# Performance work log

Measured on AMD Instinct MI355X. Metric: run time of the kernel, lower is better.

The kernel has to match this reference:

```python
import jax, jax.numpy as jnp
import numpy as np

N_LEADS = 12

def _norm_adj():
    """Normalized adjacency matching GCNConv semantics on the fixed ECG graph.
    The buffer adj already includes eye(12); PyG GCNConv (add_self_loops=True)
    adds one more self-loop of weight 1, so effective self-weight is 2.
    A_norm = D^{-1/2} A_eff D^{-1/2}.
    """
    adj = np.zeros((N_LEADS, N_LEADS), dtype=np.float32)
    conns = [(0, 1), (0, 2), (1, 2), (0, 3), (1, 3), (2, 3), (0, 4), (1, 4), (1, 5), (2, 5),
             (6, 7), (7, 8), (8, 9), (9, 10), (10, 11)]
    for i, j in conns:
        adj[i, j] = 1.0
        adj[j, i] = 1.0
    a_eff = adj + 2.0 * np.eye(N_LEADS, dtype=np.float32)  # buffer eye + PyG self-loop
    deg = a_eff.sum(axis=1)
    dinv = 1.0 / np.sqrt(deg)
    return jnp.asarray(dinv[:, None] * a_eff * dinv[None, :])

A_NORM = _norm_adj()  # (12, 12)

def setup_inputs() -> dict:
    key = jax.random.key(0)
    ks = jax.random.split(key, 7)
    B, F_IN, H, OUT = 16384, 512, 256, 128
    s = 0.02
    return {
        "x": jax.random.normal(ks[0], (B, N_LEADS, F_IN), dtype=jnp.float32),
        "W1": jax.random.normal(ks[1], (F_IN, H), dtype=jnp.float32) * s,
        "b1": jnp.zeros((H,), dtype=jnp.float32),
        "W2": jax.random.normal(ks[2], (H, H), dtype=jnp.float32) * s,
        "b2": jnp.zeros((H,), dtype=jnp.float32),
        "W3": jax.random.normal(ks[3], (H, OUT), dtype=jnp.float32) * s,
        "b3": jnp.zeros((OUT,), dtype=jnp.float32),
    }

def _gcn(a, x, w, b):
    # GCNConv: A_norm @ (X W) + b, batched over b. Shapes: x (B,12,f), w (f,o)
    return jnp.einsum("nm,bmo->bno", a, jnp.einsum("bnf,fo->bno", x, w)) + b

def reference(x, W1, b1, W2, b2, W3, b3):
    a = A_NORM.astype(x.dtype)
    h = jax.nn.relu(_gcn(a, x, W1, b1))   # dropout is identity in eval mode
    h = jax.nn.relu(_gcn(a, h, W2, b2))
    h = _gcn(a, h, W3, b3)                # (B, 12, out)
    x_mean = h.mean(axis=1)
    x_max = h.max(axis=1)
    return jnp.concatenate([x_mean, x_max], axis=1)  # (B, 2*out)
```

## Files before the change

kernel.cpp:

```cpp
#include <hip/hip_runtime.h>
#include <math.h>

typedef _Float16 f16x8 __attribute__((ext_vector_type(8)));
typedef _Float16 f16x2 __attribute__((ext_vector_type(2)));
typedef float    f32x4 __attribute__((ext_vector_type(4)));

namespace {
constexpr unsigned kMask[12] = {0x01Eu,0x03Du,0x02Bu,0x007u,0x003u,0x006u,
                                0x080u,0x140u,0x280u,0x500u,0xA00u,0x400u};
constexpr float kDinv[12] = {
    0.40824829046386302f, 0.37796447300922720f, 0.40824829046386302f,
    0.44721359549995794f, 0.5f, 0.5f,
    0.57735026918962576f, 0.5f, 0.5f, 0.5f, 0.5f, 0.57735026918962576f};

constexpr int ROWS = 48;
constexpr int AST  = 72;
constexpr int HST  = 258;
constexpr int ABYTES = ROWS * AST * 2;
constexpr int HBYTES = ROWS * HST * 2;
constexpr int SMEM   = ABYTES + HBYTES;
}

__device__ __forceinline__ void barrier_keep_vmcnt()
{
    __builtin_amdgcn_sched_barrier(0);
    asm volatile("s_waitcnt lgkmcnt(0)" ::: "memory");
    __builtin_amdgcn_s_barrier();
    __builtin_amdgcn_sched_barrier(0);
}

template<int R0>
__device__ __forceinline__ void mix_rows(const float2 (&y)[12],
                                         _Float16* __restrict__ Abuf,
                                         int g, int f2)
{
    #pragma unroll
    for (int i = 0; i < 3; ++i) {
        const int r = R0 + i;
        float sx = 2.0f * y[r].x;
        float sy = 2.0f * y[r].y;
        #pragma unroll
        for (int j = 0; j < 12; ++j)
            if ((kMask[r] >> j) & 1u) { sx += y[j].x; sy += y[j].y; }
        sx *= kDinv[r]; sy *= kDinv[r];
        f16x2 h2; h2.x = (_Float16)sx; h2.y = (_Float16)sy;
        *(f16x2*)&Abuf[(g*12 + r)*AST + f2*2] = h2;
    }
}

template<int K, int N, bool SRC_LDS>
__device__ __forceinline__ void run_layer(
    const float*    __restrict__ xg,
    const _Float16* __restrict__ hs,
    const _Float16* __restrict__ wt,
    _Float16* __restrict__ Abuf,
    long rowbase, int tid,
    f32x4 (&acc)[3][N/128])
{
    constexpr int NT = N / 128, KC = K / 64;
    const int lane = tid & 63, wave = tid >> 6;
    const int l15 = lane & 15, q = lane >> 4;
    const int g   = (tid >> 5) & 3;
    const int f2  = tid & 31;
    const int qtr = tid >> 7;

    #pragma unroll
    for (int a = 0; a < 3; ++a)
        #pragma unroll
        for (int b = 0; b < NT; ++b)
            acc[a][b] = (f32x4){0.f, 0.f, 0.f, 0.f};

    float2 y[12];
    if constexpr (!SRC_LDS) {
        #pragma unroll
        for (int n = 0; n < 12; ++n) {
            const float* p = xg + (rowbase + g*12 + n) * (long)K + f2*2;
            y[n].x = kDinv[n] * p[0]; y[n].y = kDinv[n] * p[1];
        }
    }

    for (int kc = 0; kc < KC; ++kc) {
        f16x8 bf[2][NT];
        #pragma unroll
        for (int ks = 0; ks < 2; ++ks)
            #pragma unroll
            for (int tn = 0; tn < NT; ++tn)
                bf[ks][tn] = *(const f16x8*)(wt
                    + (long)(wave*NT*16 + tn*16 + l15) * K
                    + kc*64 + ks*32 + q*8);

        if constexpr (SRC_LDS) {
            #pragma unroll
            for (int n = 0; n < 12; ++n) {
                const f16x2 h2 = *(const f16x2*)&hs[(g*12 + n)*HST + kc*64 + f2*2];
                y[n].x = kDinv[n] * (float)h2.x;
                y[n].y = kDinv[n] * (float)h2.y;
            }
        }
        switch (qtr) {
            case 0:  mix_rows<0>(y, Abuf, g, f2); break;
            case 1:  mix_rows<3>(y, Abuf, g, f2); break;
            case 2:  mix_rows<6>(y, Abuf, g, f2); break;
            default: mix_rows<9>(y, Abuf, g, f2); break;
        }

        if constexpr (!SRC_LDS) {
            if (kc + 1 < KC) {
                #pragma unroll
                for (int n = 0; n < 12; ++n) {
                    const float* p = xg + (rowbase + g*12 + n) * (long)K
                                        + (kc + 1)*64 + f2*2;
                    y[n].x = kDinv[n] * p[0]; y[n].y = kDinv[n] * p[1];
                }
            }
        }
        barrier_keep_vmcnt();

        #pragma unroll
        for (int ks = 0; ks < 2; ++ks) {
            f16x8 af[3];
            #pragma unroll
            for (int tm = 0; tm < 3; ++tm)
                af[tm] = *(const f16x8*)&Abuf[(tm*16 + l15)*AST + ks*32 + q*8];
            #pragma unroll
            for (int tm = 0; tm < 3; ++tm)
                #pragma unroll
                for (int tn = 0; tn < NT; ++tn)
                    acc[tm][tn] = __builtin_amdgcn_mfma_f32_16x16x32_f16(
                        af[tm], bf[ks][tn], acc[tm][tn], 0, 0, 0);
        }
        barrier_keep_vmcnt();
    }
}

template<int N>
__device__ __forceinline__ void store_h(
    f32x4 (&acc)[3][N/128], const float* __restrict__ bias,
    _Float16* __restrict__ H, int tid)
{
    constexpr int NT = N / 128;
    const int lane = tid & 63, wave = tid >> 6;
    const int l15 = lane & 15, q = lane >> 4;
    float bcol[NT];
    #pragma unroll
    for (int tn = 0; tn < NT; ++tn) bcol[tn] = bias[wave*NT*16 + tn*16 + l15];
    #pragma unroll
    for (int tm = 0; tm < 3; ++tm)
        #pragma unroll
        for (int tn = 0; tn < NT; ++tn)
            #pragma unroll
            for (int r = 0; r < 4; ++r) {
                const int row = tm*16 + q*4 + r;
                const int col = wave*NT*16 + tn*16 + l15;
                H[row*HST + col] = (_Float16)fmaxf(acc[tm][tn][r] + bcol[tn], 0.f);
            }
}

__global__ __launch_bounds__(512, 4)
void gcn_fused(const float* __restrict__ x,
               const _Float16* __restrict__ wt1, const float* __restrict__ b1,
               const _Float16* __restrict__ wt2, const float* __restrict__ b2,
               const _Float16* __restrict__ wt3, const float* __restrict__ b3,
               float* __restrict__ out)
{
    __shared__ __align__(16) char smem[SMEM];
    _Float16* Abuf = (_Float16*)smem;
    _Float16* Hbuf = (_Float16*)(smem + ABYTES);

    const int tid = threadIdx.x;
    const long rowbase = (long)blockIdx.x * ROWS;

    f32x4 acc[3][2];
    run_layer<512, 256, false>(x, nullptr, wt1, Abuf, rowbase, tid, acc);
    store_h<256>(acc, b1, Hbuf, tid);
    __syncthreads();

    run_layer<256, 256, true>(nullptr, Hbuf, wt2, Abuf, rowbase, tid, acc);
    store_h<256>(acc, b2, Hbuf, tid);
    __syncthreads();

    f32x4 acc3[3][1];
    run_layer<256, 128, true>(nullptr, Hbuf, wt3, Abuf, rowbase, tid, acc3);

    float* C = (float*)smem;
    {
        const int lane = tid & 63, wave = tid >> 6;
        const int l15 = lane & 15, q = lane >> 4;
        #pragma unroll
        for (int tm = 0; tm < 3; ++tm)
            #pragma unroll
            for (int r = 0; r < 4; ++r) {
                const int row = tm*16 + q*4 + r;
                const int col = wave*16 + l15;
                C[row*129 + col] = acc3[tm][0][r];
            }
    }
    __syncthreads();
    {
        const int bl  = tid >> 7;
        const int col = tid & 127;
        float s = 0.0f, mx = -INFINITY;
        #pragma unroll
        for (int n = 0; n < 12; ++n) {
            const float v = C[(bl*12 + n)*129 + col];
            s += v; mx = fmaxf(mx, v);
        }
        const float b  = b3[col];
        const long  ob = ((long)blockIdx.x*4 + bl) * 256;
        out[ob + col]       = s / 12.0f + b;
        out[ob + 128 + col] = mx + b;
    }
}

__global__ void prep_weights(const float* __restrict__ W1,
                             const float* __restrict__ W2,
                             const float* __restrict__ W3,
                             _Float16* __restrict__ wt)
{
    const int tid = blockIdx.x * 256 + threadIdx.x;
    constexpr int N1 = 512*256, N2 = 256*256, N3 = 256*128;
    if (tid < N1) {
        const int o = tid >> 9, k = tid & 511;
        wt[tid] = (_Float16)W1[k*256 + o];
    } else if (tid < N1 + N2) {
        const int t = tid - N1;
        const int o = t >> 8, k = t & 255;
        wt[N1 + t] = (_Float16)W2[k*256 + o];
    } else if (tid < N1 + N2 + N3) {
        const int t = tid - N1 - N2;
        const int o = t >> 8, k = t & 255;
        wt[N1 + N2 + t] = (_Float16)W3[k*128 + o];
    }
}

extern "C" void kernel_launch(void* const* d_in, const int* in_sizes, int n_in,
                              void* d_out, int out_size, void* d_ws, size_t ws_size,
                              hipStream_t stream)
{
    const float* x  = (const float*)d_in[0];
    const float* W1 = (const float*)d_in[1];
    const float* b1 = (const float*)d_in[2];
    const float* W2 = (const float*)d_in[3];
    const float* b2 = (const float*)d_in[4];
    const float* W3 = (const float*)d_in[5];
    const float* b3 = (const float*)d_in[6];
    float* out = (float*)d_out;

    _Float16* wt  = (_Float16*)d_ws;
    _Float16* wt1 = wt;
    _Float16* wt2 = wt + 512*256;
    _Float16* wt3 = wt + 512*256 + 256*256;

    prep_weights<<<896, 256, 0, stream>>>(W1, W2, W3, wt);
    gcn_fused<<<4096, 512, 0, stream>>>(x, wt1, b1, wt2, b2, wt3, b3, out);
}
```

Before: 745.5 us.

## Double-buffer A tiles, double rows per block, split graph mixing by component

New measurement: 602.2 us. 1.24x faster.

```diff
diff --git a/kernel.cpp b/kernel.cpp
--- a/kernel.cpp
+++ b/kernel.cpp
@@ -6,17 +6,16 @@
 typedef float    f32x4 __attribute__((ext_vector_type(4)));
 
 namespace {
-constexpr unsigned kMask[12] = {0x01Eu,0x03Du,0x02Bu,0x007u,0x003u,0x006u,
-                                0x080u,0x140u,0x280u,0x500u,0xA00u,0x400u};
 constexpr float kDinv[12] = {
     0.40824829046386302f, 0.37796447300922720f, 0.40824829046386302f,
     0.44721359549995794f, 0.5f, 0.5f,
     0.57735026918962576f, 0.5f, 0.5f, 0.5f, 0.5f, 0.57735026918962576f};
 
-constexpr int ROWS = 48;
-constexpr int AST  = 72;
-constexpr int HST  = 258;
-constexpr int ABYTES = ROWS * AST * 2;
+constexpr int ROWS  = 96;
+constexpr int AST   = 72;
+constexpr int AHALF = ROWS * AST;
+constexpr int ABYTES = 2 * AHALF * 2;
+constexpr int HST   = 258;
 constexpr int HBYTES = ROWS * HST * 2;
 constexpr int SMEM   = ABYTES + HBYTES;
 }
@@ -29,129 +28,177 @@
     __builtin_amdgcn_sched_barrier(0);
 }
 
-template<int R0>
-__device__ __forceinline__ void mix_rows(const float2 (&y)[12],
-                                         _Float16* __restrict__ Abuf,
-                                         int g, int f2)
-{
-    #pragma unroll
-    for (int i = 0; i < 3; ++i) {
-        const int r = R0 + i;
-        float sx = 2.0f * y[r].x;
-        float sy = 2.0f * y[r].y;
-        #pragma unroll
-        for (int j = 0; j < 12; ++j)
-            if ((kMask[r] >> j) & 1u) { sx += y[j].x; sy += y[j].y; }
-        sx *= kDinv[r]; sy *= kDinv[r];
-        f16x2 h2; h2.x = (_Float16)sx; h2.y = (_Float16)sy;
-        *(f16x2*)&Abuf[(g*12 + r)*AST + f2*2] = h2;
-    }
+template<int K, bool SRC_LDS, bool CB>
+__device__ __forceinline__ void load_y(const float* __restrict__ xrow,
+                                       const _Float16* __restrict__ hs,
+                                       int g, int f2, int kc, float2 (&y)[6])
+{
+    #pragma unroll
+    for (int n = 0; n < 6; ++n) {
+        const float d = kDinv[(CB ? 6 : 0) + n];
+        if constexpr (!SRC_LDS) {
+            const float* p = xrow + (long)n * K + kc * 64;
+            y[n].x = d * p[0];
+            y[n].y = d * p[1];
+        } else {
+            const f16x2 h2 = *(const f16x2*)&hs[(g*12 + (CB?6:0) + n)*HST + kc*64 + f2*2];
+            y[n].x = d * (float)h2.x;
+            y[n].y = d * (float)h2.y;
+        }
+    }
+}
+
+template<bool CB>
+__device__ __forceinline__ void mix6(const float2 (&y)[6],
+                                     _Float16* __restrict__ A, int g, int f2)
+{
+    float rx[6], ry[6];
+    if constexpr (!CB) {
+        rx[0] = 2.f*y[0].x + y[1].x + y[2].x + y[3].x + y[4].x;
+        ry[0] = 2.f*y[0].y + y[1].y + y[2].y + y[3].y + y[4].y;
+        rx[1] = 2.f*y[1].x + y[0].x + y[2].x + y[3].x + y[4].x + y[5].x;
+        ry[1] = 2.f*y[1].y + y[0].y + y[2].y + y[3].y + y[4].y + y[5].y;
+        rx[2] = 2.f*y[2].x + y[0].x + y[1].x + y[3].x + y[5].x;
+        ry[2] = 2.f*y[2].y + y[0].y + y[1].y + y[3].y + y[5].y;
+        rx[3] = 2.f*y[3].x + y[0].x + y[1].x + y[2].x;
+        ry[3] = 2.f*y[3].y + y[0].y + y[1].y + y[2].y;
+        rx[4] = 2.f*y[4].x + y[0].x + y[1].x;
+        ry[4] = 2.f*y[4].y + y[0].y + y[1].y;
+        rx[5] = 2.f*y[5].x + y[1].x + y[2].x;
+        ry[5] = 2.f*y[5].y + y[1].y + y[2].y;
+    } else {
+        rx[0] = 2.f*y[0].x + y[1].x;
+        ry[0] = 2.f*y[0].y + y[1].y;
+        rx[1] = 2.f*y[1].x + y[0].x + y[2].x;
+        ry[1] = 2.f*y[1].y + y[0].y + y[2].y;
+        rx[2] = 2.f*y[2].x + y[1].x + y[3].x;
+        ry[2] = 2.f*y[2].y + y[1].y + y[3].y;
+        rx[3] = 2.f*y[3].x + y[2].x + y[4].x;
+        ry[3] = 2.f*y[3].y + y[2].y + y[4].y;
+        rx[4] = 2.f*y[4].x + y[3].x + y[5].x;
+        ry[4] = 2.f*y[4].y + y[3].y + y[5].y;
+        rx[5] = 2.f*y[5].x + y[4].x;
+        ry[5] = 2.f*y[5].y + y[4].y;
+    }
+    #pragma unroll
+    for (int i = 0; i < 6; ++i) {
+        const float d = kDinv[(CB ? 6 : 0) + i];
+        f16x2 h2;
+        h2.x = (_Float16)(d * rx[i]);
+        h2.y = (_Float16)(d * ry[i]);
+        *(f16x2*)&A[(g*12 + (CB?6:0) + i)*AST + f2*2] = h2;
+    }
+}
+
+template<int K, int N, bool SRC_LDS>
+__device__ __forceinline__ void layer_iter(
+    const float* __restrict__ xrow, const _Float16* __restrict__ hs,
+    const _Float16* __restrict__ wtl,
+    const _Float16* __restrict__ AbufR, _Float16* __restrict__ AbufW,
+    bool cb, int g, int f2, int kc, int l15, int q,
+    float2 (&yCons)[6], float2 (&yFill)[6],
+    f32x4 (&acc)[6][N/128])
+{
+    constexpr int NTW = N / 128, KC = K / 64;
+
+    f16x8 bf[2][NTW];
+    #pragma unroll
+    for (int ks = 0; ks < 2; ++ks)
+        #pragma unroll
+        for (int tn = 0; tn < NTW; ++tn)
+            bf[ks][tn] = *(const f16x8*)(wtl + (long)tn*16*K + kc*64 + ks*32);
+
+    if (cb) {
+        if constexpr (!SRC_LDS)
+            if (kc + 2 < KC) load_y<K,false,true>(xrow, hs, g, f2, kc+2, yFill);
+        if (kc + 1 < KC) {
+            if constexpr (SRC_LDS) load_y<K,true,true>(xrow, hs, g, f2, kc+1, yCons);
+            mix6<true>(yCons, AbufW, g, f2);
+        }
+    } else {
+        if constexpr (!SRC_LDS)
+            if (kc + 2 < KC) load_y<K,false,false>(xrow, hs, g, f2, kc+2, yFill);
+        if (kc + 1 < KC) {
+            if constexpr (SRC_LDS) load_y<K,true,false>(xrow, hs, g, f2, kc+1, yCons);
+            mix6<false>(yCons, AbufW, g, f2);
+        }
+    }
+
+    #pragma unroll
+    for (int ks = 0; ks < 2; ++ks)
+        #pragma unroll
+        for (int tm = 0; tm < 6; ++tm) {
+            const f16x8 af = *(const f16x8*)&AbufR[(tm*16 + l15)*AST + ks*32 + q*8];
+            #pragma unroll
+            for (int tn = 0; tn < NTW; ++tn)
+                acc[tm][tn] = __builtin_amdgcn_mfma_f32_16x16x32_f16(
+                    af, bf[ks][tn], acc[tm][tn], 0, 0, 0);
+        }
+    barrier_keep_vmcnt();
 }
 
 template<int K, int N, bool SRC_LDS>
 __device__ __forceinline__ void run_layer(
-    const float*    __restrict__ xg,
-    const _Float16* __restrict__ hs,
-    const _Float16* __restrict__ wt,
-    _Float16* __restrict__ Abuf,
-    long rowbase, int tid,
-    f32x4 (&acc)[3][N/128])
-{
-    constexpr int NT = N / 128, KC = K / 64;
+    const float* __restrict__ xg, const _Float16* __restrict__ hs,
+    const _Float16* __restrict__ wt, _Float16* __restrict__ Abuf,
+    long rowbase, int tid, f32x4 (&acc)[6][N/128])
+{
+    constexpr int NTW = N / 128, KC = K / 64;
     const int lane = tid & 63, wave = tid >> 6;
     const int l15 = lane & 15, q = lane >> 4;
-    const int g   = (tid >> 5) & 3;
-    const int f2  = tid & 31;
-    const int qtr = tid >> 7;
-
-    #pragma unroll
-    for (int a = 0; a < 3; ++a)
-        #pragma unroll
-        for (int b = 0; b < NT; ++b)
+    const bool cb = tid >= 256;
+    const int mi = tid & 255, g = mi >> 5, f2 = mi & 31;
+
+    const float* xrow = nullptr;
+    if constexpr (!SRC_LDS)
+        xrow = xg + (rowbase + g*12 + (cb ? 6 : 0)) * (long)K + f2*2;
+    const _Float16* wtl = wt + (long)(wave*NTW*16 + l15) * K + q*8;
+
+    #pragma unroll
+    for (int a = 0; a < 6; ++a)
+        #pragma unroll
+        for (int b = 0; b < NTW; ++b)
             acc[a][b] = (f32x4){0.f, 0.f, 0.f, 0.f};
 
-    float2 y[12];
-    if constexpr (!SRC_LDS) {
-        #pragma unroll
-        for (int n = 0; n < 12; ++n) {
-            const float* p = xg + (rowbase + g*12 + n) * (long)K + f2*2;
-            y[n].x = kDinv[n] * p[0]; y[n].y = kDinv[n] * p[1];
-        }
-    }
-
-    for (int kc = 0; kc < KC; ++kc) {
-        f16x8 bf[2][NT];
-        #pragma unroll
-        for (int ks = 0; ks < 2; ++ks)
-            #pragma unroll
-            for (int tn = 0; tn < NT; ++tn)
-                bf[ks][tn] = *(const f16x8*)(wt
-                    + (long)(wave*NT*16 + tn*16 + l15) * K
-                    + kc*64 + ks*32 + q*8);
-
-        if constexpr (SRC_LDS) {
-            #pragma unroll
-            for (int n = 0; n < 12; ++n) {
-                const f16x2 h2 = *(const f16x2*)&hs[(g*12 + n)*HST + kc*64 + f2*2];
-                y[n].x = kDinv[n] * (float)h2.x;
-                y[n].y = kDinv[n] * (float)h2.y;
-            }
-        }
-        switch (qtr) {
-            case 0:  mix_rows<0>(y, Abuf, g, f2); break;
-            case 1:  mix_rows<3>(y, Abuf, g, f2); break;
-            case 2:  mix_rows<6>(y, Abuf, g, f2); break;
-            default: mix_rows<9>(y, Abuf, g, f2); break;
-        }
-
-        if constexpr (!SRC_LDS) {
-            if (kc + 1 < KC) {
-                #pragma unroll
-                for (int n = 0; n < 12; ++n) {
-                    const float* p = xg + (rowbase + g*12 + n) * (long)K
-                                        + (kc + 1)*64 + f2*2;
-                    y[n].x = kDinv[n] * p[0]; y[n].y = kDinv[n] * p[1];
-                }
-            }
-        }
-        barrier_keep_vmcnt();
-
-        #pragma unroll
-        for (int ks = 0; ks < 2; ++ks) {
-            f16x8 af[3];
-            #pragma unroll
-            for (int tm = 0; tm < 3; ++tm)
-                af[tm] = *(const f16x8*)&Abuf[(tm*16 + l15)*AST + ks*32 + q*8];
-            #pragma unroll
-            for (int tm = 0; tm < 3; ++tm)
-                #pragma unroll
-                for (int tn = 0; tn < NT; ++tn)
-                    acc[tm][tn] = __builtin_amdgcn_mfma_f32_16x16x32_f16(
-                        af[tm], bf[ks][tn], acc[tm][tn], 0, 0, 0);
-        }
-        barrier_keep_vmcnt();
+    float2 yA[6], yB[6];
+    if (cb) {
+        load_y<K,SRC_LDS,true>(xrow, hs, g, f2, 0, yA);
+        if constexpr (!SRC_LDS) load_y<K,false,true>(xrow, hs, g, f2, 1, yB);
+        mix6<true>(yA, Abuf, g, f2);
+    } else {
+        load_y<K,SRC_LDS,false>(xrow, hs, g, f2, 0, yA);
+        if constexpr (!SRC_LDS) load_y<K,false,false>(xrow, hs, g, f2, 1, yB);
+        mix6<false>(yA, Abuf, g, f2);
+    }
+    barrier_keep_vmcnt();
+
+    for (int kc = 0; kc < KC; kc += 2) {
+        layer_iter<K,N,SRC_LDS>(xrow, hs, wtl, Abuf,         Abuf + AHALF,
+                                cb, g, f2, kc,     l15, q, yB, yA, acc);
+        layer_iter<K,N,SRC_LDS>(xrow, hs, wtl, Abuf + AHALF, Abuf,
+                                cb, g, f2, kc + 1, l15, q, yA, yB, acc);
     }
 }
 
 template<int N>
 __device__ __forceinline__ void store_h(
-    f32x4 (&acc)[3][N/128], const float* __restrict__ bias,
+    f32x4 (&acc)[6][N/128], const float* __restrict__ bias,
     _Float16* __restrict__ H, int tid)
 {
-    constexpr int NT = N / 128;
+    constexpr int NTW = N / 128;
     const int lane = tid & 63, wave = tid >> 6;
     const int l15 = lane & 15, q = lane >> 4;
-    float bcol[NT];
-    #pragma unroll
-    for (int tn = 0; tn < NT; ++tn) bcol[tn] = bias[wave*NT*16 + tn*16 + l15];
-    #pragma unroll
-    for (int tm = 0; tm < 3; ++tm)
-        #pragma unroll
-        for (int tn = 0; tn < NT; ++tn)
+    float bcol[NTW];
+    #pragma unroll
+    for (int tn = 0; tn < NTW; ++tn) bcol[tn] = bias[wave*NTW*16 + tn*16 + l15];
+    #pragma unroll
+    for (int tm = 0; tm < 6; ++tm)
+        #pragma unroll
+        for (int tn = 0; tn < NTW; ++tn)
             #pragma unroll
             for (int r = 0; r < 4; ++r) {
                 const int row = tm*16 + q*4 + r;
-                const int col = wave*NT*16 + tn*16 + l15;
+                const int col = wave*NTW*16 + tn*16 + l15;
                 H[row*HST + col] = (_Float16)fmaxf(acc[tm][tn][r] + bcol[tn], 0.f);
             }
 }
@@ -170,7 +217,7 @@
     const int tid = threadIdx.x;
     const long rowbase = (long)blockIdx.x * ROWS;
 
-    f32x4 acc[3][2];
+    f32x4 acc[6][2];
     run_layer<512, 256, false>(x, nullptr, wt1, Abuf, rowbase, tid, acc);
     store_h<256>(acc, b1, Hbuf, tid);
     __syncthreads();
@@ -179,7 +226,7 @@
     store_h<256>(acc, b2, Hbuf, tid);
     __syncthreads();
 
-    f32x4 acc3[3][1];
+    f32x4 acc3[6][1];
     run_layer<256, 128, true>(nullptr, Hbuf, wt3, Abuf, rowbase, tid, acc3);
 
     float* C = (float*)smem;
@@ -187,18 +234,17 @@
         const int lane = tid & 63, wave = tid >> 6;
         const int l15 = lane & 15, q = lane >> 4;
         #pragma unroll
-        for (int tm = 0; tm < 3; ++tm)
+        for (int tm = 0; tm < 6; ++tm)
             #pragma unroll
-            for (int r = 0; r < 4; ++r) {
-                const int row = tm*16 + q*4 + r;
-                const int col = wave*16 + l15;
-                C[row*129 + col] = acc3[tm][0][r];
-            }
+            for (int r = 0; r < 4; ++r)
+                C[(tm*16 + q*4 + r)*129 + wave*16 + l15] = acc3[tm][0][r];
     }
     __syncthreads();
-    {
-        const int bl  = tid >> 7;
-        const int col = tid & 127;
+    #pragma unroll
+    for (int p = 0; p < 2; ++p) {
+        const int idx = tid + p*512;
+        const int bl  = idx >> 7;
+        const int col = idx & 127;
         float s = 0.0f, mx = -INFINITY;
         #pragma unroll
         for (int n = 0; n < 12; ++n) {
@@ -206,7 +252,7 @@
             s += v; mx = fmaxf(mx, v);
         }
         const float b  = b3[col];
-        const long  ob = ((long)blockIdx.x*4 + bl) * 256;
+        const long  ob = ((long)blockIdx.x*8 + bl) * 256;
         out[ob + col]       = s / 12.0f + b;
         out[ob + 128 + col] = mx + b;
     }
@@ -252,5 +298,5 @@
     _Float16* wt3 = wt + 512*256 + 256*256;
 
     prep_weights<<<896, 256, 0, stream>>>(W1, W2, W3, wt);
-    gcn_fused<<<4096, 512, 0, stream>>>(x, wt1, b1, wt2, b2, wt3, b3, out);
-}
+    gcn_fused<<<2048, 512, 0, stream>>>(x, wt1, b1, wt2, b2, wt3, b3, out);
+}
```
